# Optimization experiments

Hardware: AMD Instinct MI355X
Metric: run time of the kernel (lower is better)

The kernel has to match this reference:

```python
import jax, jax.numpy as jnp
import numpy as np

# geomloss SamplesLoss('sinkhorn', p=2, blur=0.05, diameter=4.0, scaling=0.5, debias=True)
P_EXP = 2.0
BLUR = 0.05
DIAMETER = 4.0
SCALING = 0.5


def eps_schedule():
    # geomloss epsilon_schedule: annealed temperatures from diameter^p down to blur^p
    mids = [np.exp(e) for e in np.arange(P_EXP * np.log(DIAMETER), P_EXP * np.log(BLUR), P_EXP * np.log(SCALING))]
    return [float(DIAMETER ** P_EXP)] + [float(e) for e in mids] + [float(BLUR ** P_EXP)]


def sq_cost(x, y):
    # C[b,i,j] = 0.5 * ||x_bi - y_bj||^2   (geomloss p=2 cost)
    x2 = jnp.sum(x * x, axis=-1)[:, :, None]   # [B,N,1]
    y2 = jnp.sum(y * y, axis=-1)[:, None, :]   # [B,1,M]
    return 0.5 * (x2 + y2) - jnp.einsum('bid,bjd->bij', x, y)


def softmin(eps, C, h):
    # h: [B,M] dual log-potential; C: [B,N,M] -> [B,N]
    return -eps * jax.nn.logsumexp(h[:, None, :] - C / eps, axis=2)


def sinkhorn_divergence(x, y):
    B, N, _ = x.shape
    M = y.shape[1]
    dt = x.dtype
    a_log = jnp.full((B, N), -np.log(N), dtype=dt)  # uniform weights (log)
    b_log = jnp.full((B, M), -np.log(M), dtype=dt)

    C_xy = sq_cost(x, y)
    C_yx = sq_cost(y, x)
    C_xx = sq_cost(x, x)
    C_yy = sq_cost(y, y)

    eps_list = eps_schedule()
    eps = eps_list[0]
    # initialization (damping = 1 for balanced OT)
    a_x = softmin(eps, C_xx, a_log)
    b_y = softmin(eps, C_yy, b_log)
    b_x = softmin(eps, C_xy, b_log)
    a_y = softmin(eps, C_yx, a_log)

    # eps-scaling descent with symmetrized updates (runs under no_grad in geomloss)
    for eps in eps_list:
        at_y = softmin(eps, C_yx, a_log + b_x / eps)
        bt_x = softmin(eps, C_xy, b_log + a_y / eps)
        at_x = softmin(eps, C_xx, a_log + a_x / eps)
        bt_y = softmin(eps, C_yy, b_log + b_y / eps)
        a_y, b_x = 0.5 * (a_y + at_y), 0.5 * (b_x + bt_x)
        a_x, b_y = 0.5 * (a_x + at_x), 0.5 * (b_y + bt_y)

    # last extrapolation: gradients flow only through the cost matrices here
    eps = eps_list[-1]
    sg = jax.lax.stop_gradient
    a_y, b_x = (softmin(eps, C_yx, sg(a_log + b_x / eps)),
                softmin(eps, C_xy, sg(b_log + a_y / eps)))
    a_x = softmin(eps, C_xx, sg(a_log + a_x / eps))
    b_y = softmin(eps, C_yy, sg(b_log + b_y / eps))

    a = jnp.exp(a_log)
    b = jnp.exp(b_log)
    # debiased Sinkhorn cost per batch, then torch.sum over batch as in forward()
    F = jnp.sum(a * (b_x - a_x), axis=-1) + jnp.sum(b * (a_y - b_y), axis=-1)
    return jnp.sum(F)


def setup_inputs() -> dict:
    key = jax.random.key(0)
    k1, k2 = jax.random.split(key)
    true_data = jax.random.normal(k1, (2, 4096, 3), dtype=jnp.float32)
    particles = jax.random.normal(k2, (2, 4096, 3), dtype=jnp.float32)
    return {"true_data": true_data, "particles": particles}


def reference(true_data, particles):
    # rm_map is identity here: y = rm_map(particles) = particles
    return sinkhorn_divergence(true_data, particles)
```

## Files before the change

### kernel.cpp

```cpp
#include <hip/hip_runtime.h>


typedef __attribute__((ext_vector_type(8))) short short8;
typedef __attribute__((ext_vector_type(8))) __bf16 bf16x8;
typedef __attribute__((ext_vector_type(4))) float f32x4;
typedef __attribute__((ext_vector_type(2))) float f32x2;

#define NPT 4096
#define BLOCK 512
#define COLS 1024
#define GRID 512
#define NLAUNCH 11
#define EXP2 __builtin_amdgcn_exp2f
#define LOG2 __builtin_amdgcn_logf
#define KLOG2E 1.4426950408889634f
#define KLN2 0.6931471805599453f

__device__ const float epsC[NLAUNCH] = {16.0f, 16.0f, 16.0f, 4.0f, 1.0f, 0.25f,
                                        0.0625f, 0.015625f, 0.00390625f, 0.0025f, 0.0025f};

__device__ inline unsigned short f2bf(float f) {
  unsigned u = __float_as_uint(f);
  return (unsigned short)((u + 0x7FFF + ((u >> 16) & 1)) >> 16);
}
__device__ inline float bf2f(unsigned short h) {
  return __uint_as_float(((unsigned)h) << 16);
}

__device__ inline float2 ldP(const float2* p) {
  unsigned long long v = __hip_atomic_load((const unsigned long long*)p,
                                           __ATOMIC_RELAXED, __HIP_MEMORY_SCOPE_AGENT);
  return __builtin_bit_cast(float2, v);
}
__device__ inline void stP(float2* p, float2 f) {
  __hip_atomic_store((unsigned long long*)p, __builtin_bit_cast(unsigned long long, f),
                     __ATOMIC_RELAXED, __HIP_MEMORY_SCOPE_AGENT);
}
__device__ inline float ldF(const float* p) {
  unsigned v = __hip_atomic_load((const unsigned*)p, __ATOMIC_RELAXED,
                                 __HIP_MEMORY_SCOPE_AGENT);
  return __uint_as_float(v);
}
__device__ inline void stF(float* p, float f) {
  __hip_atomic_store((unsigned*)p, __float_as_uint(f), __ATOMIC_RELAXED,
                     __HIP_MEMORY_SCOPE_AGENT);
}

struct PArgs {
  const float* x;
  const float* y;
  float2* P0;
  float2* P1;
  float* F0;
  float* F1;
  unsigned* slots;
  unsigned* release;
};

__device__ inline void grid_barrier(unsigned* slots, unsigned* release, unsigned epoch) {
  __syncthreads();
  if (threadIdx.x == 0)
    __hip_atomic_store(&slots[blockIdx.x], epoch, __ATOMIC_RELAXED,
                       __HIP_MEMORY_SCOPE_AGENT);
  if (blockIdx.x == 0) {
    unsigned spins = 0;
    int ok;
    do {
      unsigned v = __hip_atomic_load(&slots[threadIdx.x], __ATOMIC_RELAXED,
                                     __HIP_MEMORY_SCOPE_AGENT);
      ok = (v >= epoch) || (spins > (1u << 20));
      if (!ok) __builtin_amdgcn_s_sleep(1);
      ++spins;
    } while (!__syncthreads_and(ok));
    if (threadIdx.x == 0)
      __hip_atomic_store(release, epoch, __ATOMIC_RELAXED, __HIP_MEMORY_SCOPE_AGENT);
    __syncthreads();
  } else {
    if (threadIdx.x == 0) {
      unsigned spins = 0;
      while (__hip_atomic_load(release, __ATOMIC_RELAXED,
                               __HIP_MEMORY_SCOPE_AGENT) < epoch) {
        __builtin_amdgcn_s_sleep(2);
        if (++spins > (1u << 22)) break;
      }
    }
    __syncthreads();
  }
}

__device__ inline void lse_merge16(float& m, float& s,
                                   f32x4 c0, f32x4 c1, f32x4 c2, f32x4 c3) {
  float t0 = fmaxf(fmaxf(c0.x, c0.y), c0.z);
  float t1 = fmaxf(fmaxf(c0.w, c1.x), c1.y);
  float t2 = fmaxf(fmaxf(c1.z, c1.w), c2.x);
  float t3 = fmaxf(fmaxf(c2.y, c2.z), c2.w);
  float t4 = fmaxf(fmaxf(c3.x, c3.y), c3.z);
  float u0 = fmaxf(fmaxf(t0, t1), c3.w);
  float u1 = fmaxf(fmaxf(t2, t3), t4);
  float cm = fmaxf(u0, u1);
  float mn = fmaxf(m, cm);
  float sc = EXP2(m - mn);
  f32x2 mn2 = {mn, mn};
  f32x2 sa = {0.0f, 0.0f}, sb = {0.0f, 0.0f};
  f32x2 d;
  d = (f32x2){c0.x, c0.y} - mn2; sa += (f32x2){EXP2(d.x), EXP2(d.y)};
  d = (f32x2){c0.z, c0.w} - mn2; sb += (f32x2){EXP2(d.x), EXP2(d.y)};
  d = (f32x2){c1.x, c1.y} - mn2; sa += (f32x2){EXP2(d.x), EXP2(d.y)};
  d = (f32x2){c1.z, c1.w} - mn2; sb += (f32x2){EXP2(d.x), EXP2(d.y)};
  d = (f32x2){c2.x, c2.y} - mn2; sa += (f32x2){EXP2(d.x), EXP2(d.y)};
  d = (f32x2){c2.z, c2.w} - mn2; sb += (f32x2){EXP2(d.x), EXP2(d.y)};
  d = (f32x2){c3.x, c3.y} - mn2; sa += (f32x2){EXP2(d.x), EXP2(d.y)};
  d = (f32x2){c3.z, c3.w} - mn2; sb += (f32x2){EXP2(d.x), EXP2(d.y)};
  sa += sb;
  s = fmaf(s, sc, sa.x + sa.y);
  m = mn;
}

__global__ __launch_bounds__(BLOCK, 4) void softmin_persist(PArgs A) {
  __shared__ short8 fragA0[COLS];
  __shared__ short8 fragA1[COLS];

  const int bid  = blockIdx.x;
  const int tbl  = bid >> 6;
  const int task = tbl >> 1, batch = tbl & 1;
  const int rem  = bid & 63;
  const int part = rem >> 4;
  const int rc   = rem & 15;

  const bool rowIsX = (task == 0) | (task == 2);
  const bool colIsX = (task == 1) | (task == 2);
  const float* xp = (rowIsX ? A.x : A.y) + batch * NPT * 3;
  const float* yp = (colIsX ? A.x : A.y) + batch * NPT * 3;

  const float hc = -8.317766166719343f;
  const int pidxA[4] = {1, 0, 2, 3};
  const int tP = pidxA[task] * 2 + batch;

  const int lane = threadIdx.x & 63;
  const int wave = threadIdx.x >> 6;
  const int q    = lane >> 4;
  const int rowbase = rc * 256 + wave * 32;

  bf16x8 Bf[2];
#pragma unroll
  for (int rs = 0; rs < 2; ++rs) {
    int i = rowbase + rs * 16 + (lane & 15);
    float X0 = xp[3 * i], X1 = xp[3 * i + 1], X2 = xp[3 * i + 2];
    unsigned short xh0 = f2bf(X0), xh1 = f2bf(X1), xh2 = f2bf(X2);
    unsigned short xl0 = f2bf(X0 - bf2f(xh0));
    unsigned short xl1 = f2bf(X1 - bf2f(xh1));
    unsigned short xl2 = f2bf(X2 - bf2f(xh2));
    short8 bb = (short8)0;
    if (q == 0) {
      short8 t = {(short)xh0, (short)xh1, (short)xh2,
                  (short)xh0, (short)xh1, (short)xh2,
                  (short)xl0, (short)xl1};
      bb = t;
    } else if (q == 1) {
      short8 t = {(short)xl2, (short)0x3F80, (short)0x3F80, (short)0x3F80,
                  (short)xl0, (short)xl1, (short)xl2, 0};
      bb = t;
    }
    Bf[rs] = __builtin_bit_cast(bf16x8, bb);
  }

  float Y0[2], Y1[2], Y2[2], Y2N[2];
#pragma unroll
  for (int c = 0; c < 2; ++c) {
    int j = part * COLS + threadIdx.x + c * BLOCK;
    Y0[c] = yp[3 * j]; Y1[c] = yp[3 * j + 1]; Y2[c] = yp[3 * j + 2];
    Y2N[c] = 0.5f * (Y0[c] * Y0[c] + Y1[c] * Y1[c] + Y2[c] * Y2[c]);
  }

  float epsPrev = 1.0f;
  for (int L = 0; L < NLAUNCH; ++L) {
    const float eps = epsC[L];
    const int usePot  = (L >= 1);
    const int avgPrev = (L >= 2);
    const float2* Pprev = (L & 1) ? A.P0 : A.P1;
    float2*       Pcur  = (L & 1) ? A.P1 : A.P0;
    const float*  Fprev = (L & 1) ? A.F0 : A.F1;
    float*        Fcur  = (L & 1) ? A.F1 : A.F0;
    const float inv_eps = 1.0f / eps;
    const float sY = inv_eps * KLOG2E;

#pragma unroll
    for (int c = 0; c < 2; ++c) {
      int jl = threadIdx.x + c * BLOCK;
      int j  = part * COLS + jl;
      float y0 = Y0[c], y1 = Y1[c], y2 = Y2[c];
      float y2n = Y2N[c];
      float pot = 0.0f;
      if (usePot) {
        float2 q0 = ldP(&Pprev[(tP * 4 + 0) * NPT + j]);
        float2 q1 = ldP(&Pprev[(tP * 4 + 1) * NPT + j]);
        float2 q2 = ldP(&Pprev[(tP * 4 + 2) * NPT + j]);
        float2 q3 = ldP(&Pprev[(tP * 4 + 3) * NPT + j]);
        float M = fmaxf(fmaxf(q0.x, q1.x), fmaxf(q2.x, q3.x));
        float S = q0.y * EXP2(q0.x - M) + q1.y * EXP2(q1.x - M)
                + q2.y * EXP2(q2.x - M) + q3.y * EXP2(q3.x - M);
        float Lg = M + LOG2(S);
        float r = y2n - epsPrev * KLN2 * Lg;
        if (avgPrev) r = 0.5f * (ldF(&Fprev[tP * NPT + j]) + r);
        pot = r;
        if (rc == 0) stF(&Fcur[tP * NPT + j], pot);
      }
      float T = (hc + (pot - y2n) * inv_eps) * KLOG2E;
      float s0 = y0 * sY, s1 = y1 * sY, s2 = y2 * sY;
      unsigned short yh0 = f2bf(s0), yh1 = f2bf(s1), yh2 = f2bf(s2);
      unsigned short yl0 = f2bf(s0 - bf2f(yh0));
      unsigned short yl1 = f2bf(s1 - bf2f(yh1));
      unsigned short yl2 = f2bf(s2 - bf2f(yh2));
      unsigned short Th = f2bf(T);
      float tr = T - bf2f(Th);
      unsigned short Tm = f2bf(tr);
      tr -= bf2f(Tm);
      unsigned short Tl = f2bf(tr);
      short8 h0 = {(short)yh0, (short)yh1, (short)yh2,
                   (short)yl0, (short)yl1, (short)yl2,
                   (short)yh0, (short)yh1};
      short8 h1 = {(short)yh2, (short)Th, (short)Tm, (short)Tl,
                   (short)yl0, (short)yl1, (short)yl2, 0};
      fragA0[jl] = h0;
      fragA1[jl] = h1;
    }
    __syncthreads();

    const short8* srcA = (lane & 16) ? fragA1 : fragA0;
    const int colsel = lane & 15;
    const f32x4 Z = {0.0f, 0.0f, 0.0f, 0.0f};
    short8 as0 = (short8)0, as1 = (short8)0, as2 = (short8)0, as3 = (short8)0;
    float m0 = -__builtin_inff(), s0_ = 0.0f;
    float m1 = -__builtin_inff(), s1_ = 0.0f;

    for (int jt = 0; jt < COLS / 16; jt += 4) {
      if (lane < 32) {
        as0 = srcA[(jt + 0) * 16 + colsel];
        as1 = srcA[(jt + 1) * 16 + colsel];
        as2 = srcA[(jt + 2) * 16 + colsel];
        as3 = srcA[(jt + 3) * 16 + colsel];
      }
      bf16x8 A0 = __builtin_bit_cast(bf16x8, as0);
      bf16x8 A1 = __builtin_bit_cast(bf16x8, as1);
      bf16x8 A2 = __builtin_bit_cast(bf16x8, as2);
      bf16x8 A3 = __builtin_bit_cast(bf16x8, as3);
      f32x4 c00 = __builtin_amdgcn_mfma_f32_16x16x32_bf16(A0, Bf[0], Z, 0, 0, 0);
      f32x4 c01 = __builtin_amdgcn_mfma_f32_16x16x32_bf16(A1, Bf[0], Z, 0, 0, 0);
      f32x4 c02 = __builtin_amdgcn_mfma_f32_16x16x32_bf16(A2, Bf[0], Z, 0, 0, 0);
      f32x4 c03 = __builtin_amdgcn_mfma_f32_16x16x32_bf16(A3, Bf[0], Z, 0, 0, 0);
      f32x4 c10 = __builtin_amdgcn_mfma_f32_16x16x32_bf16(A0, Bf[1], Z, 0, 0, 0);
      f32x4 c11 = __builtin_amdgcn_mfma_f32_16x16x32_bf16(A1, Bf[1], Z, 0, 0, 0);
      f32x4 c12 = __builtin_amdgcn_mfma_f32_16x16x32_bf16(A2, Bf[1], Z, 0, 0, 0);
      f32x4 c13 = __builtin_amdgcn_mfma_f32_16x16x32_bf16(A3, Bf[1], Z, 0, 0, 0);
      lse_merge16(m0, s0_, c00, c01, c02, c03);
      lse_merge16(m1, s1_, c10, c11, c12, c13);
    }

#pragma unroll
    for (int rs = 0; rs < 2; ++rs) {
      float m = rs ? m1 : m0;
      float s = rs ? s1_ : s0_;
#pragma unroll
      for (int off = 16; off <= 32; off <<= 1) {
        float mo = __shfl_xor(m, off, 64);
        float so = __shfl_xor(s, off, 64);
        float mn = fmaxf(m, mo);
        s = s * EXP2(m - mn) + so * EXP2(mo - mn);
        m = mn;
      }
      if (lane < 16) {
        int i = rowbase + rs * 16 + lane;
        stP(&Pcur[(tbl * 4 + part) * NPT + i], make_float2(m, s));
      }
    }

    epsPrev = eps;
    if (L < NLAUNCH - 1)
      grid_barrier(A.slots, A.release, (unsigned)(L + 1));
  }
}

__global__ __launch_bounds__(256) void reduce1(const float2* P, float* R1) {
  int u = blockIdx.x * 256 + threadIdx.x;
  int b = u >> 12, i = u & 4095;
  float Ls[4];
#pragma unroll
  for (int t = 0; t < 4; ++t) {
    int tbl = t * 2 + b;
    float2 q0 = P[(tbl * 4 + 0) * NPT + i];
    float2 q1 = P[(tbl * 4 + 1) * NPT + i];
    float2 q2 = P[(tbl * 4 + 2) * NPT + i];
    float2 q3 = P[(tbl * 4 + 3) * NPT + i];
    float M = fmaxf(fmaxf(q0.x, q1.x), fmaxf(q2.x, q3.x));
    float S = q0.y * EXP2(q0.x - M) + q1.y * EXP2(q1.x - M)
            + q2.y * EXP2(q2.x - M) + q3.y * EXP2(q3.x - M);
    Ls[t] = M + LOG2(S);
  }
  float acc = (Ls[0] - Ls[2]) + (Ls[1] - Ls[3]);
#pragma unroll
  for (int off = 32; off >= 1; off >>= 1) acc += __shfl_xor(acc, off, 64);
  __shared__ float red[4];
  int wave = threadIdx.x >> 6, lane = threadIdx.x & 63;
  if (lane == 0) red[wave] = acc;
  __syncthreads();
  if (threadIdx.x == 0)
    R1[blockIdx.x] = red[0] + red[1] + red[2] + red[3];
}

__global__ __launch_bounds__(64) void reduce2(const float* R1, float* out) {
  float a = (threadIdx.x < 32) ? R1[threadIdx.x] : 0.0f;
#pragma unroll
  for (int off = 32; off >= 1; off >>= 1) a += __shfl_xor(a, off, 64);
  if (threadIdx.x == 0)
    out[0] = a * (-0.0025f * KLN2 / 4096.0f);
}

extern "C" void kernel_launch(void* const* d_in, const int* in_sizes, int n_in,
                              void* d_out, int out_size, void* d_ws, size_t ws_size,
                              hipStream_t stream) {
  const float* x = (const float*)d_in[0];
  const float* y = (const float*)d_in[1];
  float* out = (float*)d_out;
  float* W = (float*)d_ws;

  PArgs A;
  A.x = x;
  A.y = y;
  A.P0 = (float2*)W;
  A.P1 = (float2*)(W + 262144);
  A.F0 = W + 524288;
  A.F1 = W + 557056;
  float* R1buf = W + 589824;
  A.slots   = (unsigned*)(W + 590080);
  A.release = (unsigned*)(W + 590592);

  hipMemsetAsync((void*)A.slots, 0, 513 * sizeof(unsigned), stream);

  softmin_persist<<<dim3(GRID), dim3(BLOCK), 0, stream>>>(A);

  reduce1<<<32, 256, 0, stream>>>(A.P0, R1buf);
  reduce2<<<1, 64, 0, stream>>>(R1buf, out);
}
```

Before: 323.5 us.

## Split column range into eight parts and double persistent grid to 1024 blocks

The persistent softmin kernel now splits the 4096 columns into eight 512-column parts instead of four 1024-column parts, which doubles the grid to 1024 blocks and raises launch bounds to 8 blocks per CU. Each block does half the per-iteration column work, and the potential merge and final reduction combine eight partial (max, sum) pairs instead of four. The grid barrier now polls two slots per thread. The intent is better occupancy and latency hiding across the CUs. The cost is more partial-result traffic and a more expensive barrier, and co-residency of all 1024 blocks requires 8 blocks per CU to fit, otherwise the barrier falls back to its spin timeouts.

New measurement: 382.2 us. +18.1%, slower.

```diff
diff --git a/kernel.cpp b/kernel.cpp
--- a/kernel.cpp
+++ b/kernel.cpp
@@ -8,8 +8,10 @@
 
 #define NPT 4096
 #define BLOCK 512
-#define COLS 1024
-#define GRID 512
+#define COLS 512
+#define NPARTS 8
+#define NRC 16
+#define GRID 1024
 #define NLAUNCH 11
 #define EXP2 __builtin_amdgcn_exp2f
 #define LOG2 __builtin_amdgcn_logf
@@ -66,9 +68,11 @@
     unsigned spins = 0;
     int ok;
     do {
-      unsigned v = __hip_atomic_load(&slots[threadIdx.x], __ATOMIC_RELAXED,
-                                     __HIP_MEMORY_SCOPE_AGENT);
-      ok = (v >= epoch) || (spins > (1u << 20));
+      unsigned v0 = __hip_atomic_load(&slots[threadIdx.x], __ATOMIC_RELAXED,
+                                      __HIP_MEMORY_SCOPE_AGENT);
+      unsigned v1 = __hip_atomic_load(&slots[threadIdx.x + BLOCK], __ATOMIC_RELAXED,
+                                      __HIP_MEMORY_SCOPE_AGENT);
+      ok = ((v0 >= epoch) & (v1 >= epoch)) || (spins > (1u << 20));
       if (!ok) __builtin_amdgcn_s_sleep(1);
       ++spins;
     } while (!__syncthreads_and(ok));
@@ -116,14 +120,14 @@
   m = mn;
 }
 
-__global__ __launch_bounds__(BLOCK, 4) void softmin_persist(PArgs A) {
+__global__ __launch_bounds__(BLOCK, 8) void softmin_persist(PArgs A) {
   __shared__ short8 fragA0[COLS];
   __shared__ short8 fragA1[COLS];
 
   const int bid  = blockIdx.x;
-  const int tbl  = bid >> 6;
+  const int tbl  = bid >> 7;
   const int task = tbl >> 1, batch = tbl & 1;
-  const int rem  = bid & 63;
+  const int rem  = bid & 127;
   const int part = rem >> 4;
   const int rc   = rem & 15;
 
@@ -164,13 +168,9 @@
     Bf[rs] = __builtin_bit_cast(bf16x8, bb);
   }
 
-  float Y0[2], Y1[2], Y2[2], Y2N[2];
-#pragma unroll
-  for (int c = 0; c < 2; ++c) {
-    int j = part * COLS + threadIdx.x + c * BLOCK;
-    Y0[c] = yp[3 * j]; Y1[c] = yp[3 * j + 1]; Y2[c] = yp[3 * j + 2];
-    Y2N[c] = 0.5f * (Y0[c] * Y0[c] + Y1[c] * Y1[c] + Y2[c] * Y2[c]);
-  }
+  const int jcol = part * COLS + threadIdx.x;
+  const float Y0 = yp[3 * jcol], Y1 = yp[3 * jcol + 1], Y2 = yp[3 * jcol + 2];
+  const float Y2N = 0.5f * (Y0 * Y0 + Y1 * Y1 + Y2 * Y2);
 
   float epsPrev = 1.0f;
   for (int L = 0; L < NLAUNCH; ++L) {
@@ -184,29 +184,33 @@
     const float inv_eps = 1.0f / eps;
     const float sY = inv_eps * KLOG2E;
 
-#pragma unroll
-    for (int c = 0; c < 2; ++c) {
-      int jl = threadIdx.x + c * BLOCK;
-      int j  = part * COLS + jl;
-      float y0 = Y0[c], y1 = Y1[c], y2 = Y2[c];
-      float y2n = Y2N[c];
+    {
+      const int jl = threadIdx.x;
+      const int j  = jcol;
       float pot = 0.0f;
       if (usePot) {
-        float2 q0 = ldP(&Pprev[(tP * 4 + 0) * NPT + j]);
-        float2 q1 = ldP(&Pprev[(tP * 4 + 1) * NPT + j]);
-        float2 q2 = ldP(&Pprev[(tP * 4 + 2) * NPT + j]);
-        float2 q3 = ldP(&Pprev[(tP * 4 + 3) * NPT + j]);
-        float M = fmaxf(fmaxf(q0.x, q1.x), fmaxf(q2.x, q3.x));
-        float S = q0.y * EXP2(q0.x - M) + q1.y * EXP2(q1.x - M)
-                + q2.y * EXP2(q2.x - M) + q3.y * EXP2(q3.x - M);
+        float2 qq0 = ldP(&Pprev[(tP * 8 + 0) * NPT + j]);
+        float2 qq1 = ldP(&Pprev[(tP * 8 + 1) * NPT + j]);
+        float2 qq2 = ldP(&Pprev[(tP * 8 + 2) * NPT + j]);
+        float2 qq3 = ldP(&Pprev[(tP * 8 + 3) * NPT + j]);
+        float2 qq4 = ldP(&Pprev[(tP * 8 + 4) * NPT + j]);
+        float2 qq5 = ldP(&Pprev[(tP * 8 + 5) * NPT + j]);
+        float2 qq6 = ldP(&Pprev[(tP * 8 + 6) * NPT + j]);
+        float2 qq7 = ldP(&Pprev[(tP * 8 + 7) * NPT + j]);
+        float M = fmaxf(fmaxf(fmaxf(qq0.x, qq1.x), fmaxf(qq2.x, qq3.x)),
+                        fmaxf(fmaxf(qq4.x, qq5.x), fmaxf(qq6.x, qq7.x)));
+        float S = qq0.y * EXP2(qq0.x - M) + qq1.y * EXP2(qq1.x - M)
+                + qq2.y * EXP2(qq2.x - M) + qq3.y * EXP2(qq3.x - M)
+                + qq4.y * EXP2(qq4.x - M) + qq5.y * EXP2(qq5.x - M)
+                + qq6.y * EXP2(qq6.x - M) + qq7.y * EXP2(qq7.x - M);
         float Lg = M + LOG2(S);
-        float r = y2n - epsPrev * KLN2 * Lg;
+        float r = Y2N - epsPrev * KLN2 * Lg;
         if (avgPrev) r = 0.5f * (ldF(&Fprev[tP * NPT + j]) + r);
         pot = r;
         if (rc == 0) stF(&Fcur[tP * NPT + j], pot);
       }
-      float T = (hc + (pot - y2n) * inv_eps) * KLOG2E;
-      float s0 = y0 * sY, s1 = y1 * sY, s2 = y2 * sY;
+      float T = (hc + (pot - Y2N) * inv_eps) * KLOG2E;
+      float s0 = Y0 * sY, s1 = Y1 * sY, s2 = Y2 * sY;
       unsigned short yh0 = f2bf(s0), yh1 = f2bf(s1), yh2 = f2bf(s2);
       unsigned short yl0 = f2bf(s0 - bf2f(yh0));
       unsigned short yl1 = f2bf(s1 - bf2f(yh1));
@@ -270,7 +274,7 @@
       }
       if (lane < 16) {
         int i = rowbase + rs * 16 + lane;
-        stP(&Pcur[(tbl * 4 + part) * NPT + i], make_float2(m, s));
+        stP(&Pcur[(tbl * 8 + part) * NPT + i], make_float2(m, s));
       }
     }
 
@@ -287,13 +291,14 @@
 #pragma unroll
   for (int t = 0; t < 4; ++t) {
     int tbl = t * 2 + b;
-    float2 q0 = P[(tbl * 4 + 0) * NPT + i];
-    float2 q1 = P[(tbl * 4 + 1) * NPT + i];
-    float2 q2 = P[(tbl * 4 + 2) * NPT + i];
-    float2 q3 = P[(tbl * 4 + 3) * NPT + i];
-    float M = fmaxf(fmaxf(q0.x, q1.x), fmaxf(q2.x, q3.x));
-    float S = q0.y * EXP2(q0.x - M) + q1.y * EXP2(q1.x - M)
-            + q2.y * EXP2(q2.x - M) + q3.y * EXP2(q3.x - M);
+    float2 qq[8];
+#pragma unroll
+    for (int p = 0; p < 8; ++p) qq[p] = P[(tbl * 8 + p) * NPT + i];
+    float M = fmaxf(fmaxf(fmaxf(qq[0].x, qq[1].x), fmaxf(qq[2].x, qq[3].x)),
+                    fmaxf(fmaxf(qq[4].x, qq[5].x), fmaxf(qq[6].x, qq[7].x)));
+    float S = 0.0f;
+#pragma unroll
+    for (int p = 0; p < 8; ++p) S += qq[p].y * EXP2(qq[p].x - M);
     Ls[t] = M + LOG2(S);
   }
   float acc = (Ls[0] - Ls[2]) + (Ls[1] - Ls[3]);
@@ -327,14 +332,14 @@
   A.x = x;
   A.y = y;
   A.P0 = (float2*)W;
-  A.P1 = (float2*)(W + 262144);
-  A.F0 = W + 524288;
-  A.F1 = W + 557056;
-  float* R1buf = W + 589824;
-  A.slots   = (unsigned*)(W + 590080);
-  A.release = (unsigned*)(W + 590592);
-
-  hipMemsetAsync((void*)A.slots, 0, 513 * sizeof(unsigned), stream);
+  A.P1 = (float2*)(W + 524288);
+  A.F0 = W + 1048576;
+  A.F1 = W + 1081344;
+  float* R1buf = W + 1114112;
+  A.slots   = (unsigned*)(W + 1114144);
+  A.release = (unsigned*)(W + 1115168);
+
+  hipMemsetAsync((void*)A.slots, 0, 1025 * sizeof(unsigned), stream);
 
   softmin_persist<<<dim3(GRID), dim3(BLOCK), 0, stream>>>(A);
 
```

## Double block size to 1024 threads with one 16-row tile per wave

Applied to the files above, without the earlier changes.

Raises the persistent kernel's block size from 512 to 1024 threads, so each wave handles one 16-row MFMA tile instead of two and each thread stages one column instead of two. The grid barrier now guards its slot polling so that only the first GRID threads read slots. The intent is more waves per CU to hide the exp2/LSE latency, with lower per-thread register pressure. The cost is that each LDS A-fragment is loaded once per 16 rows instead of per 32, doubling LDS traffic per MFMA, and 1024-thread blocks make the occupancy and co-residency of the persistent grid harder to guarantee.

Measured after the change: 330.4 us. +2.1%, slower.

```diff
diff --git a/kernel.cpp b/kernel.cpp
--- a/kernel.cpp
+++ b/kernel.cpp
@@ -7,7 +7,7 @@
 typedef __attribute__((ext_vector_type(2))) float f32x2;
 
 #define NPT 4096
-#define BLOCK 512
+#define BLOCK 1024
 #define COLS 1024
 #define GRID 512
 #define NLAUNCH 11
@@ -66,10 +66,13 @@
     unsigned spins = 0;
     int ok;
     do {
-      unsigned v = __hip_atomic_load(&slots[threadIdx.x], __ATOMIC_RELAXED,
-                                     __HIP_MEMORY_SCOPE_AGENT);
-      ok = (v >= epoch) || (spins > (1u << 20));
-      if (!ok) __builtin_amdgcn_s_sleep(1);
+      ok = 1;
+      if (threadIdx.x < GRID) {
+        unsigned v = __hip_atomic_load(&slots[threadIdx.x], __ATOMIC_RELAXED,
+                                       __HIP_MEMORY_SCOPE_AGENT);
+        ok = (v >= epoch) || (spins > (1u << 20));
+        if (!ok) __builtin_amdgcn_s_sleep(1);
+      }
       ++spins;
     } while (!__syncthreads_and(ok));
     if (threadIdx.x == 0)
@@ -116,7 +119,7 @@
   m = mn;
 }
 
-__global__ __launch_bounds__(BLOCK, 4) void softmin_persist(PArgs A) {
+__global__ __launch_bounds__(BLOCK, 8) void softmin_persist(PArgs A) {
   __shared__ short8 fragA0[COLS];
   __shared__ short8 fragA1[COLS];
 
@@ -139,12 +142,11 @@
   const int lane = threadIdx.x & 63;
   const int wave = threadIdx.x >> 6;
   const int q    = lane >> 4;
-  const int rowbase = rc * 256 + wave * 32;
-
-  bf16x8 Bf[2];
-#pragma unroll
-  for (int rs = 0; rs < 2; ++rs) {
-    int i = rowbase + rs * 16 + (lane & 15);
+  const int rowbase = rc * 256 + wave * 16;
+
+  bf16x8 Bf;
+  {
+    int i = rowbase + (lane & 15);
     float X0 = xp[3 * i], X1 = xp[3 * i + 1], X2 = xp[3 * i + 2];
     unsigned short xh0 = f2bf(X0), xh1 = f2bf(X1), xh2 = f2bf(X2);
     unsigned short xl0 = f2bf(X0 - bf2f(xh0));
@@ -161,16 +163,12 @@
                   (short)xl0, (short)xl1, (short)xl2, 0};
       bb = t;
     }
-    Bf[rs] = __builtin_bit_cast(bf16x8, bb);
+    Bf = __builtin_bit_cast(bf16x8, bb);
   }
 
-  float Y0[2], Y1[2], Y2[2], Y2N[2];
-#pragma unroll
-  for (int c = 0; c < 2; ++c) {
-    int j = part * COLS + threadIdx.x + c * BLOCK;
-    Y0[c] = yp[3 * j]; Y1[c] = yp[3 * j + 1]; Y2[c] = yp[3 * j + 2];
-    Y2N[c] = 0.5f * (Y0[c] * Y0[c] + Y1[c] * Y1[c] + Y2[c] * Y2[c]);
-  }
+  const int jcol = part * COLS + threadIdx.x;
+  const float Y0 = yp[3 * jcol], Y1 = yp[3 * jcol + 1], Y2 = yp[3 * jcol + 2];
+  const float Y2N = 0.5f * (Y0 * Y0 + Y1 * Y1 + Y2 * Y2);
 
   float epsPrev = 1.0f;
   for (int L = 0; L < NLAUNCH; ++L) {
@@ -184,12 +182,9 @@
     const float inv_eps = 1.0f / eps;
     const float sY = inv_eps * KLOG2E;
 
-#pragma unroll
-    for (int c = 0; c < 2; ++c) {
-      int jl = threadIdx.x + c * BLOCK;
-      int j  = part * COLS + jl;
-      float y0 = Y0[c], y1 = Y1[c], y2 = Y2[c];
-      float y2n = Y2N[c];
+    {
+      const int jl = threadIdx.x;
+      const int j  = jcol;
       float pot = 0.0f;
       if (usePot) {
         float2 q0 = ldP(&Pprev[(tP * 4 + 0) * NPT + j]);
@@ -200,13 +195,13 @@
         float S = q0.y * EXP2(q0.x - M) + q1.y * EXP2(q1.x - M)
                 + q2.y * EXP2(q2.x - M) + q3.y * EXP2(q3.x - M);
         float Lg = M + LOG2(S);
-        float r = y2n - epsPrev * KLN2 * Lg;
+        float r = Y2N - epsPrev * KLN2 * Lg;
         if (avgPrev) r = 0.5f * (ldF(&Fprev[tP * NPT + j]) + r);
         pot = r;
         if (rc == 0) stF(&Fcur[tP * NPT + j], pot);
       }
-      float T = (hc + (pot - y2n) * inv_eps) * KLOG2E;
-      float s0 = y0 * sY, s1 = y1 * sY, s2 = y2 * sY;
+      float T = (hc + (pot - Y2N) * inv_eps) * KLOG2E;
+      float s0 = Y0 * sY, s1 = Y1 * sY, s2 = Y2 * sY;
       unsigned short yh0 = f2bf(s0), yh1 = f2bf(s1), yh2 = f2bf(s2);
       unsigned short yl0 = f2bf(s0 - bf2f(yh0));
       unsigned short yl1 = f2bf(s1 - bf2f(yh1));
@@ -231,7 +226,6 @@
     const f32x4 Z = {0.0f, 0.0f, 0.0f, 0.0f};
     short8 as0 = (short8)0, as1 = (short8)0, as2 = (short8)0, as3 = (short8)0;
     float m0 = -__builtin_inff(), s0_ = 0.0f;
-    float m1 = -__builtin_inff(), s1_ = 0.0f;
 
     for (int jt = 0; jt < COLS / 16; jt += 4) {
       if (lane < 32) {
@@ -244,22 +238,16 @@
       bf16x8 A1 = __builtin_bit_cast(bf16x8, as1);
       bf16x8 A2 = __builtin_bit_cast(bf16x8, as2);
       bf16x8 A3 = __builtin_bit_cast(bf16x8, as3);
-      f32x4 c00 = __builtin_amdgcn_mfma_f32_16x16x32_bf16(A0, Bf[0], Z, 0, 0, 0);
-      f32x4 c01 = __builtin_amdgcn_mfma_f32_16x16x32_bf16(A1, Bf[0], Z, 0, 0, 0);
-      f32x4 c02 = __builtin_amdgcn_mfma_f32_16x16x32_bf16(A2, Bf[0], Z, 0, 0, 0);
-      f32x4 c03 = __builtin_amdgcn_mfma_f32_16x16x32_bf16(A3, Bf[0], Z, 0, 0, 0);
-      f32x4 c10 = __builtin_amdgcn_mfma_f32_16x16x32_bf16(A0, Bf[1], Z, 0, 0, 0);
-      f32x4 c11 = __builtin_amdgcn_mfma_f32_16x16x32_bf16(A1, Bf[1], Z, 0, 0, 0);
-      f32x4 c12 = __builtin_amdgcn_mfma_f32_16x16x32_bf16(A2, Bf[1], Z, 0, 0, 0);
-      f32x4 c13 = __builtin_amdgcn_mfma_f32_16x16x32_bf16(A3, Bf[1], Z, 0, 0, 0);
+      f32x4 c00 = __builtin_amdgcn_mfma_f32_16x16x32_bf16(A0, Bf, Z, 0, 0, 0);
+      f32x4 c01 = __builtin_amdgcn_mfma_f32_16x16x32_bf16(A1, Bf, Z, 0, 0, 0);
+      f32x4 c02 = __builtin_amdgcn_mfma_f32_16x16x32_bf16(A2, Bf, Z, 0, 0, 0);
+      f32x4 c03 = __builtin_amdgcn_mfma_f32_16x16x32_bf16(A3, Bf, Z, 0, 0, 0);
       lse_merge16(m0, s0_, c00, c01, c02, c03);
-      lse_merge16(m1, s1_, c10, c11, c12, c13);
-    }
-
-#pragma unroll
-    for (int rs = 0; rs < 2; ++rs) {
-      float m = rs ? m1 : m0;
-      float s = rs ? s1_ : s0_;
+    }
+
+    {
+      float m = m0;
+      float s = s0_;
 #pragma unroll
       for (int off = 16; off <= 32; off <<= 1) {
         float mo = __shfl_xor(m, off, 64);
@@ -269,7 +257,7 @@
         m = mn;
       }
       if (lane < 16) {
-        int i = rowbase + rs * 16 + lane;
+        int i = rowbase + lane;
         stP(&Pcur[(tbl * 4 + part) * NPT + i], make_float2(m, s));
       }
     }
```
